# Kernel optimization log

Measured on AMD Instinct MI355X. Metric: run time of the kernel, lower is better.

## Reference

```python
import jax, jax.numpy as jnp
import numpy as np


def setup_inputs() -> dict:
    key = jax.random.key(0)
    k = jax.random.split(key, 6)
    B, S, d, n = 4, 4096, 1024, 64
    x = jax.random.normal(k[0], (B, S, d), dtype=jnp.float32)
    gate_W = jax.random.normal(k[1], (d, n), dtype=jnp.float32) / np.sqrt(d).astype(np.float32)
    gate_b = jnp.full((n,), 3.0, dtype=jnp.float32)  # nn.init.constant_(gate_proj.bias, 3.0)
    B_W = jax.random.normal(k[2], (d, n), dtype=jnp.float32) / np.sqrt(d).astype(np.float32)
    C_W = jax.random.normal(k[3], (n, d), dtype=jnp.float32) / np.sqrt(n).astype(np.float32)
    out_W = jax.random.normal(k[4], (d, d), dtype=jnp.float32) / np.sqrt(d).astype(np.float32)
    mix_weight = jnp.eye(n, dtype=jnp.float32) + 0.01 * jax.random.normal(k[5], (n, n), dtype=jnp.float32)
    return {"x": x, "gate_W": gate_W, "gate_b": gate_b, "B_W": B_W,
            "C_W": C_W, "out_W": out_W, "mix_weight": mix_weight, "chunk_size": 16}


def _ssm_forward(x, gate_W, gate_b, B_W, C_W, out_W, mix_weight, chunk_size):
    Bb, S, d = x.shape
    n = gate_W.shape[1]
    C = chunk_size
    K = S // C  # seq_len chosen divisible by chunk_size -> F.pad path is a no-op
    # Vectorized per-timestep projections (done once for the whole sequence)
    gates = jax.nn.sigmoid(jnp.einsum('bsd,dn->bsn', x, gate_W) + gate_b)  # a_t in (0,1)
    b_all = jnp.einsum('bsd,dn->bsn', x, B_W)
    a_ch = gates.reshape(Bb, K, C, n).transpose(1, 2, 0, 3)  # (K, C, B, n)
    b_ch = b_all.reshape(Bb, K, C, n).transpose(1, 2, 0, 3)

    def chunk_step(h_prev, ab):
        a_c, b_c = ab  # each (C, B, n)
        def step(h, t):
            a_t, b_t = t
            h = a_t * h + b_t
            return h, h
        h_final, h_stack = jax.lax.scan(step, h_prev, (a_c, b_c))  # h_stack: (C, B, n)
        gate_prod = jnp.prod(a_c, axis=0)  # (B, n) cumulative diag gates
        # T_chunk = mix @ diag(gate_prod): T[b,i,j] = mix[i,j] * gate_prod[b,j]
        T = mix_weight[None, :, :] * gate_prod[:, None, :]
        Th = jnp.einsum('bij,bj->bi', T, h_prev)
        b_chunk = h_final - Th
        h_next = Th + b_chunk  # canonical inter-chunk propagation: T @ h_prev + b_chunk
        return h_next, h_stack

    h0 = jnp.zeros((Bb, n), dtype=x.dtype)
    _, h_all = jax.lax.scan(chunk_step, h0, (a_ch, b_ch))  # (K, C, B, n)
    h_seq = h_all.transpose(2, 0, 1, 3).reshape(Bb, S, n)
    y = jnp.einsum('bsn,nd->bsd', h_seq, C_W)
    out_gate = jax.nn.sigmoid(jnp.einsum('bsd,de->bse', x, out_W))
    return y * out_gate


def reference(x, gate_W, gate_b, B_W, C_W, out_W, mix_weight, chunk_size):
    return _ssm_forward(x, gate_W, gate_b, B_W, C_W, out_W, mix_weight, chunk_size)
```

## Files before the change

### kernel.cpp

```cpp
#include <hip/hip_runtime.h>
#include <stdint.h>

typedef __attribute__((ext_vector_type(8))) short short8;
typedef __attribute__((ext_vector_type(4))) float f32x4;
typedef __attribute__((ext_vector_type(4))) float f4;
typedef __attribute__((ext_vector_type(4))) unsigned short us4;
typedef __attribute__((ext_vector_type(4))) unsigned int u32x4;

typedef unsigned short ushort_t;

__device__ __forceinline__ ushort_t f2bf(float f) {
    union { float f; uint32_t u; } c; c.f = f;
    uint32_t u = c.u;
    uint32_t r = u + 0x7fffu + ((u >> 16) & 1u);
    return (ushort_t)(r >> 16);
}
__device__ __forceinline__ float bf2f(ushort_t h) {
    union { uint32_t u; float f; } c; c.u = ((uint32_t)h) << 16;
    return c.f;
}
__device__ __forceinline__ uint32_t cvtpk(float lo, float hi) {
    uint32_t r;
    asm("v_cvt_pk_bf16_f32 %0, %1, %2" : "=v"(r) : "v"(lo), "v"(hi));
    return r;
}

typedef const __attribute__((address_space(1))) unsigned int as1_uint;
typedef __attribute__((address_space(3))) unsigned int as3_uint;
__device__ __forceinline__ void gload_lds16(const void* g, void* l) {
    __builtin_amdgcn_global_load_lds((as1_uint*)g, (as3_uint*)l, 16, 0, 0);
}

#define SWIDX(r, c) ((r) * 64 + ((c) ^ (((r) & 7) << 3)))

__global__ void prep_weights(const float* __restrict__ gate_W, const float* __restrict__ B_W,
                             const float* __restrict__ C_W, const float* __restrict__ out_W,
                             ushort_t* __restrict__ W1t_hi, ushort_t* __restrict__ W1t_lo,
                             ushort_t* __restrict__ outWt, ushort_t* __restrict__ Ct)
{
    int idx = blockIdx.x * 256 + threadIdx.x;
    int stride = gridDim.x * 256;
    for (int i = idx; i < 1024 * 1024; i += stride) {
        int nn = i >> 10, kk = i & 1023;
        outWt[i] = f2bf(out_W[kk * 1024 + nn]);
    }
    for (int i = idx; i < 128 * 1024; i += stride) {
        int nn = i >> 10, kk = i & 1023;
        float v = (nn < 64) ? gate_W[kk * 64 + nn] : B_W[kk * 64 + (nn - 64)];
        ushort_t h = f2bf(v);
        W1t_hi[i] = h;
        W1t_lo[i] = f2bf(v - bf2f(h));
    }
    for (int i = idx; i < 1024 * 64; i += stride) {
        int nn = i >> 6, kk = i & 63;
        Ct[i] = f2bf(C_W[kk * 1024 + nn]);
    }
}

__global__ __launch_bounds__(256, 2)
void p1_kernel(const float* __restrict__ x,
               const ushort_t* __restrict__ W1t_hi, const ushort_t* __restrict__ W1t_lo,
               ushort_t* __restrict__ x_hi, float* __restrict__ Zpart)
{
    __shared__ ushort_t Ash[128 * 64];
    __shared__ ushort_t Asl[128 * 64];
    __shared__ ushort_t Bsh[64 * 64];

    const int tid = threadIdx.x;
    const int wave = tid >> 6, lane = tid & 63;
    const int wm = wave >> 1, wn = wave & 1;
    const int s0 = blockIdx.x * 64;
    const int kc = blockIdx.y;

    f32x4 acc[4][2];
#pragma unroll
    for (int i = 0; i < 4; i++)
#pragma unroll
        for (int j = 0; j < 2; j++) { f32x4 z = {0.f,0.f,0.f,0.f}; acc[i][j] = z; }

    for (int kt = 0; kt < 8; ++kt) {
        const int k0 = kc * 512 + kt * 64;
#pragma unroll
        for (int p = 0; p < 4; ++p) {
            int c = p * 256 + wave * 64 + lane;
            int row = c >> 3, col = (c & 7) * 8;
            gload_lds16(W1t_hi + (size_t)row * 1024 + k0 + col,
                        &Ash[(p * 256 + wave * 64) * 8]);
            gload_lds16(W1t_lo + (size_t)row * 1024 + k0 + col,
                        &Asl[(p * 256 + wave * 64) * 8]);
        }
#pragma unroll
        for (int p = 0; p < 2; ++p) {
            int f = tid + p * 256;
            int row = f >> 3, col = (f & 7) * 8;
            const float* src = x + (size_t)(s0 + row) * 1024 + k0 + col;
            f4 v0 = *(const f4*)src;
            f4 v1 = *(const f4*)(src + 4);
            u32x4 pk = { cvtpk(v0[0], v0[1]), cvtpk(v0[2], v0[3]),
                         cvtpk(v1[0], v1[1]), cvtpk(v1[2], v1[3]) };
            *(u32x4*)&Bsh[row * 64 + col] = pk;
            *(u32x4*)(x_hi + (size_t)(s0 + row) * 1024 + k0 + col) = pk;
        }
        __syncthreads();
#pragma unroll
        for (int kk = 0; kk < 2; ++kk) {
            const int kb = kk * 32 + (lane >> 4) * 8;
            short8 ah[4], al[4], bh[2];
#pragma unroll
            for (int fm = 0; fm < 4; fm++) {
                int r = wm * 64 + fm * 16 + (lane & 15);
                ah[fm] = *(const short8*)&Ash[r * 64 + kb];
                al[fm] = *(const short8*)&Asl[r * 64 + kb];
            }
#pragma unroll
            for (int fn = 0; fn < 2; fn++) {
                int r = wn * 32 + fn * 16 + (lane & 15);
                bh[fn] = *(const short8*)&Bsh[r * 64 + kb];
            }
#pragma unroll
            for (int fm = 0; fm < 4; fm++)
#pragma unroll
                for (int fn = 0; fn < 2; fn++) {
                    acc[fm][fn] = __builtin_amdgcn_mfma_f32_16x16x32_bf16(ah[fm], bh[fn], acc[fm][fn], 0, 0, 0);
                    acc[fm][fn] = __builtin_amdgcn_mfma_f32_16x16x32_bf16(al[fm], bh[fn], acc[fm][fn], 0, 0, 0);
                }
        }
        __syncthreads();
    }
#pragma unroll
    for (int fm = 0; fm < 4; fm++) {
#pragma unroll
        for (int fn = 0; fn < 2; fn++) {
            int scol = s0 + wn * 32 + fn * 16 + (lane & 15);
            int b = scol >> 12, sb = scol & 4095;
            int nbase = wm * 64 + fm * 16 + ((lane >> 4) << 2);
#pragma unroll
            for (int r = 0; r < 4; r++) {
                Zpart[((size_t)kc * 512 + b * 128 + nbase + r) * 4096 + sb] = acc[fm][fn][r];
            }
        }
    }
}

__global__ __launch_bounds__(256)
void scan_kernel(const float* __restrict__ Zpart, const float* __restrict__ gate_b,
                 ushort_t* __restrict__ hT)
{
    __shared__ float SA[256], SB[256];
    const int bn = blockIdx.x;
    const int t = threadIdx.x;
    const int b = bn >> 6, n = bn & 63;
    const float gb = gate_b[n];
    const float* g0 = Zpart + ((size_t)(b * 128 + n)) * 4096;
    const float* g1 = g0 + (size_t)512 * 4096;
    const float* b0 = Zpart + ((size_t)(b * 128 + 64 + n)) * 4096;
    const float* b1 = b0 + (size_t)512 * 4096;
    const int sb = t * 16;

    float a[16], bb[16];
#pragma unroll
    for (int q = 0; q < 4; q++) {
        f4 vg0 = *(const f4*)(g0 + sb + q * 4);
        f4 vg1 = *(const f4*)(g1 + sb + q * 4);
        f4 vb0 = *(const f4*)(b0 + sb + q * 4);
        f4 vb1 = *(const f4*)(b1 + sb + q * 4);
#pragma unroll
        for (int j = 0; j < 4; j++) {
            a[q * 4 + j] = 1.f / (1.f + __expf(-(vg0[j] + vg1[j] + gb)));
            bb[q * 4 + j] = vb0[j] + vb1[j];
        }
    }
    float A = 1.f, Bv = 0.f;
#pragma unroll
    for (int i = 0; i < 16; i++) { Bv = a[i] * Bv + bb[i]; A *= a[i]; }
    SA[t] = A; SB[t] = Bv;
    __syncthreads();
    for (int off = 1; off < 256; off <<= 1) {
        float a1 = 1.f, b1v = 0.f;
        if (t >= off) { a1 = SA[t - off]; b1v = SB[t - off]; }
        float a2 = SA[t], b2 = SB[t];
        __syncthreads();
        SA[t] = a1 * a2;
        SB[t] = a2 * b1v + b2;
        __syncthreads();
    }
    float h = (t == 0) ? 0.f : SB[t - 1];
    float hv[16];
#pragma unroll
    for (int i = 0; i < 16; i++) {
        h = a[i] * h + bb[i];
        hv[i] = h;
    }
    ushort_t* dst = hT + (size_t)bn * 4096 + sb;
    u32x4 o0 = { cvtpk(hv[0], hv[1]),  cvtpk(hv[2], hv[3]),
                 cvtpk(hv[4], hv[5]),  cvtpk(hv[6], hv[7]) };
    u32x4 o1 = { cvtpk(hv[8], hv[9]),  cvtpk(hv[10], hv[11]),
                 cvtpk(hv[12], hv[13]), cvtpk(hv[14], hv[15]) };
    *(u32x4*)(dst)     = o0;
    *(u32x4*)(dst + 8) = o1;
}

__global__ __launch_bounds__(512, 2)
void gemm_out256(const ushort_t* __restrict__ x_hi, const ushort_t* __restrict__ outWt,
                 const ushort_t* __restrict__ hT, const ushort_t* __restrict__ Ct,
                 float* __restrict__ out)
{
    __shared__ ushort_t As[2][256 * 64];
    __shared__ ushort_t Bs[2][256 * 64];

    const int tid = threadIdx.x;
    const int wave = tid >> 6, lane = tid & 63;
    const int wm = wave >> 2;
    const int wn = wave & 3;

    const int flat = blockIdx.x;
    const int swz = (flat & 7) * 32 + (flat >> 3);
    const int m0 = (swz >> 2) * 256;
    const int n0 = (swz & 3) * 256;

    const int lcol0 = (lane >> 4) * 8;
    const int lrow = lane & 15;
    const int lxor = (lrow & 7) << 3;

    const int aOff0 = (wm * 32 + lrow) * 64 + (lcol0 ^ lxor);
    const int aOff1 = (wm * 32 + lrow) * 64 + ((32 + lcol0) ^ lxor);
    const int bOff0 = (wn * 64 + lrow) * 64 + (lcol0 ^ lxor);
    const int bOff1 = (wn * 64 + lrow) * 64 + ((32 + lcol0) ^ lxor);

    const int rl0 = tid >> 3;
    const int col0 = ((tid & 7) ^ (rl0 & 7)) << 3;
    const ushort_t* gB0a = outWt + (size_t)(n0 + rl0) * 1024 + col0;
    const ushort_t* gB0b = gB0a + 64 * 1024;
    const ushort_t* gB1a = outWt + (size_t)(n0 + 128 + rl0) * 1024 + col0;
    const ushort_t* gB1b = gB1a + 64 * 1024;
    const ushort_t* gA0a = x_hi + (size_t)(m0 + rl0) * 1024 + col0;
    const ushort_t* gA0b = gA0a + 64 * 1024;
    const ushort_t* gA1a = x_hi + (size_t)(m0 + 128 + rl0) * 1024 + col0;
    const ushort_t* gA1b = gA1a + 64 * 1024;

    auto STG = [&](const ushort_t*& ga, const ushort_t*& gb, ushort_t* ldsbase) {
        gload_lds16(ga, ldsbase + wave * 512);
        gload_lds16(gb, ldsbase + 4096 + wave * 512);
        ga += 64; gb += 64;
    };

    f32x4 acc[8][4];
#pragma unroll
    for (int i = 0; i < 8; i++)
#pragma unroll
        for (int j = 0; j < 4; j++) { f32x4 z = {0.f,0.f,0.f,0.f}; acc[i][j] = z; }

    STG(gB0a, gB0b, &Bs[0][0]);
    STG(gB1a, gB1b, &Bs[0][8192]);
    STG(gA0a, gA0b, &As[0][0]);
    STG(gA1a, gA1b, &As[0][8192]);
    asm volatile("s_waitcnt vmcnt(2)" ::: "memory");
    __builtin_amdgcn_s_barrier();

    short8 aR0[2][2], aR1[2][2], bfr[4][2];
#pragma unroll
    for (int mm = 0; mm < 2; ++mm) {
        aR0[mm][0] = *(const short8*)&As[0][aOff0 + mm * 1024];
        aR0[mm][1] = *(const short8*)&As[0][aOff1 + mm * 1024];
    }

#define MFMA_Q(q, AR)                                                              \
    do {                                                                           \
        __builtin_amdgcn_s_setprio(1);                                             \
        _Pragma("unroll") for (int mm = 0; mm < 2; ++mm)                           \
            _Pragma("unroll") for (int fn = 0; fn < 4; ++fn) {                     \
                acc[2*(q)+mm][fn] = __builtin_amdgcn_mfma_f32_16x16x32_bf16(       \
                    AR[mm][0], bfr[fn][0], acc[2*(q)+mm][fn], 0, 0, 0);            \
                acc[2*(q)+mm][fn] = __builtin_amdgcn_mfma_f32_16x16x32_bf16(       \
                    AR[mm][1], bfr[fn][1], acc[2*(q)+mm][fn], 0, 0, 0);            \
            }                                                                      \
        __builtin_amdgcn_s_setprio(0);                                             \
    } while (0)

    for (int t = 0; t < 16; ++t) {
        const int bc = t & 1;
        const ushort_t* as = &As[bc][0];
        const ushort_t* bs = &Bs[bc][0];
        const ushort_t* asn = &As[bc ^ 1][0];

        if (t < 15) STG(gB0a, gB0b, &Bs[bc ^ 1][0]);
#pragma unroll
        for (int fn = 0; fn < 4; ++fn) {
            bfr[fn][0] = *(const short8*)(bs + bOff0 + fn * 1024);
            bfr[fn][1] = *(const short8*)(bs + bOff1 + fn * 1024);
        }
#pragma unroll
        for (int mm = 0; mm < 2; ++mm) {
            aR1[mm][0] = *(const short8*)(as + aOff0 + 4096 + mm * 1024);
            aR1[mm][1] = *(const short8*)(as + aOff1 + 4096 + mm * 1024);
        }
        asm volatile("s_waitcnt lgkmcnt(4)" ::: "memory");
        __builtin_amdgcn_sched_barrier(0);
        MFMA_Q(0, aR0);
        if (t < 15) { asm volatile("s_waitcnt vmcnt(2)" ::: "memory"); }
        else        { asm volatile("s_waitcnt vmcnt(0)" ::: "memory"); }
        __builtin_amdgcn_s_barrier();

        if (t < 15) {
            STG(gB1a, gB1b, &Bs[bc ^ 1][8192]);
            STG(gA0a, gA0b, &As[bc ^ 1][0]);
        }
#pragma unroll
        for (int mm = 0; mm < 2; ++mm) {
            aR0[mm][0] = *(const short8*)(as + aOff0 + 2 * 4096 + mm * 1024);
            aR0[mm][1] = *(const short8*)(as + aOff1 + 2 * 4096 + mm * 1024);
        }
        asm volatile("s_waitcnt lgkmcnt(4)" ::: "memory");
        __builtin_amdgcn_sched_barrier(0);
        MFMA_Q(1, aR1);
        __builtin_amdgcn_s_barrier();

        if (t < 15) STG(gA1a, gA1b, &As[bc ^ 1][8192]);
#pragma unroll
        for (int mm = 0; mm < 2; ++mm) {
            aR1[mm][0] = *(const short8*)(as + aOff0 + 3 * 4096 + mm * 1024);
            aR1[mm][1] = *(const short8*)(as + aOff1 + 3 * 4096 + mm * 1024);
        }
        asm volatile("s_waitcnt lgkmcnt(4)" ::: "memory");
        __builtin_amdgcn_sched_barrier(0);
        MFMA_Q(2, aR0);
        if (t < 15) { asm volatile("s_waitcnt vmcnt(2)" ::: "memory"); }
        __builtin_amdgcn_s_barrier();

        if (t < 15) {
#pragma unroll
            for (int mm = 0; mm < 2; ++mm) {
                aR0[mm][0] = *(const short8*)(asn + aOff0 + mm * 1024);
                aR0[mm][1] = *(const short8*)(asn + aOff1 + mm * 1024);
            }
            asm volatile("s_waitcnt lgkmcnt(4)" ::: "memory");
        } else {
            asm volatile("s_waitcnt lgkmcnt(0)" ::: "memory");
        }
        __builtin_amdgcn_sched_barrier(0);
        MFMA_Q(3, aR1);
        __builtin_amdgcn_s_barrier();
    }
#undef MFMA_Q

    const int b64 = (m0 >> 12) * 64;
    const int sb0 = m0 & 4095;
#pragma unroll
    for (int p = 0; p < 4; ++p) {
        int c = p * 512 + wave * 64 + lane;
        int row = c >> 3;
        int col = (((c & 7) ^ (row & 7)) << 3);
        gload_lds16(Ct + (size_t)(n0 + row) * 64 + col,
                    &Bs[0][(p * 512 + wave * 64) * 8]);
    }
#pragma unroll
    for (int p = 0; p < 4; ++p) {
        int c = tid + p * 512;
        int kn = c & 63, mc = c >> 6;
        short8 v = *(const short8*)(hT + (size_t)(b64 + kn) * 4096 + sb0 + mc * 8);
#pragma unroll
        for (int j = 0; j < 8; ++j)
            As[0][SWIDX(mc * 8 + j, kn)] = (ushort_t)v[j];
    }
    __syncthreads();

    short8 by[4][2];
#pragma unroll
    for (int fn = 0; fn < 4; fn++)
#pragma unroll
        for (int kk = 0; kk < 2; kk++) {
            int r = wn * 64 + fn * 16 + lrow;
            by[fn][kk] = *(const short8*)&Bs[0][SWIDX(r, kk * 32 + lcol0)];
        }

#pragma unroll
    for (int g = 0; g < 4; g++) {
        f32x4 ty[2][4];
#pragma unroll
        for (int mm = 0; mm < 2; mm++)
#pragma unroll
            for (int fn = 0; fn < 4; fn++) { f32x4 z = {0.f,0.f,0.f,0.f}; ty[mm][fn] = z; }
#pragma unroll
        for (int mm = 0; mm < 2; mm++) {
            int r = g * 64 + wm * 32 + mm * 16 + lrow;
            short8 a0 = *(const short8*)&As[0][SWIDX(r, lcol0)];
            short8 a1 = *(const short8*)&As[0][SWIDX(r, 32 + lcol0)];
#pragma unroll
            for (int fn = 0; fn < 4; fn++) {
                ty[mm][fn] = __builtin_amdgcn_mfma_f32_16x16x32_bf16(a0, by[fn][0], ty[mm][fn], 0, 0, 0);
                ty[mm][fn] = __builtin_amdgcn_mfma_f32_16x16x32_bf16(a1, by[fn][1], ty[mm][fn], 0, 0, 0);
            }
        }
#pragma unroll
        for (int mm = 0; mm < 2; mm++)
#pragma unroll
            for (int fn = 0; fn < 4; fn++) {
                int col = n0 + wn * 64 + fn * 16 + lrow;
                int rbase = m0 + g * 64 + wm * 32 + mm * 16 + ((lane >> 4) << 2);
#pragma unroll
                for (int r = 0; r < 4; r++) {
                    float og = 1.f / (1.f + __expf(-acc[g * 2 + mm][fn][r]));
                    out[(size_t)(rbase + r) * 1024 + col] = ty[mm][fn][r] * og;
                }
            }
    }
}

extern "C" void kernel_launch(void* const* d_in, const int* in_sizes, int n_in,
                              void* d_out, int out_size, void* d_ws, size_t ws_size,
                              hipStream_t stream)
{
    const float* x      = (const float*)d_in[0];
    const float* gate_W = (const float*)d_in[1];
    const float* gate_b = (const float*)d_in[2];
    const float* B_W    = (const float*)d_in[3];
    const float* C_W    = (const float*)d_in[4];
    const float* out_W  = (const float*)d_in[5];
    float* out = (float*)d_out;

    char* ws = (char*)d_ws;
    float*    Zpart  = (float*)(ws + 0);
    ushort_t* hT     = (ushort_t*)(ws + 16777216);
    ushort_t* x_hi   = (ushort_t*)(ws + 18874368);
    ushort_t* W1t_hi = (ushort_t*)(ws + 52428800);
    ushort_t* W1t_lo = (ushort_t*)(ws + 52690944);
    ushort_t* outWt  = (ushort_t*)(ws + 52953088);
    ushort_t* Ct     = (ushort_t*)(ws + 55050240);

    prep_weights<<<512, 256, 0, stream>>>(gate_W, B_W, C_W, out_W,
                                          W1t_hi, W1t_lo, outWt, Ct);

    p1_kernel<<<dim3(256, 2), 256, 0, stream>>>(x, W1t_hi, W1t_lo, x_hi, Zpart);

    scan_kernel<<<256, 256, 0, stream>>>(Zpart, gate_b, hT);

    gemm_out256<<<256, 512, 0, stream>>>(x_hi, outWt, hT, Ct, out);
}
```

Before: 83.49 us.

## Drop split-K in projection GEMM and transpose out_W via shared-memory tiles

The projection kernel no longer splits K across two block columns. Each block now covers 32 sequence rows over the full K range, so the scan kernel reads one partial sum per gate and B value instead of adding two. Separately, the out_W transpose and bf16 conversion moves into its own kernel that goes through LDS tiles, replacing the strided global reads of the old grid-stride loop. The trade-off is that each projection block re-streams the full weight panel for half as many rows, which raises weight traffic per output row.

Result: slower. 89.85 us, median of 2 (+7.6%).

```diff
diff --git a/kernel.cpp b/kernel.cpp
--- a/kernel.cpp
+++ b/kernel.cpp
@@ -34,16 +34,12 @@
 #define SWIDX(r, c) ((r) * 64 + ((c) ^ (((r) & 7) << 3)))
 
 __global__ void prep_weights(const float* __restrict__ gate_W, const float* __restrict__ B_W,
-                             const float* __restrict__ C_W, const float* __restrict__ out_W,
+                             const float* __restrict__ C_W,
                              ushort_t* __restrict__ W1t_hi, ushort_t* __restrict__ W1t_lo,
-                             ushort_t* __restrict__ outWt, ushort_t* __restrict__ Ct)
+                             ushort_t* __restrict__ Ct)
 {
     int idx = blockIdx.x * 256 + threadIdx.x;
     int stride = gridDim.x * 256;
-    for (int i = idx; i < 1024 * 1024; i += stride) {
-        int nn = i >> 10, kk = i & 1023;
-        outWt[i] = f2bf(out_W[kk * 1024 + nn]);
-    }
     for (int i = idx; i < 128 * 1024; i += stride) {
         int nn = i >> 10, kk = i & 1023;
         float v = (nn < 64) ? gate_W[kk * 64 + nn] : B_W[kk * 64 + (nn - 64)];
@@ -57,6 +53,31 @@
     }
 }
 
+__global__ __launch_bounds__(256)
+void prep_outwt(const float* __restrict__ out_W, ushort_t* __restrict__ outWt)
+{
+    __shared__ ushort_t T[64][65];
+    const int kk0 = blockIdx.x * 64, nn0 = blockIdx.y * 64;
+    const int tid = threadIdx.x;
+#pragma unroll
+    for (int p = 0; p < 16; ++p) {
+        int r = p * 4 + (tid >> 6);
+        int c = tid & 63;
+        T[c][r] = f2bf(out_W[(size_t)(kk0 + r) * 1024 + nn0 + c]);
+    }
+    __syncthreads();
+#pragma unroll
+    for (int p = 0; p < 2; ++p) {
+        int idx = tid + p * 256;
+        int r = idx >> 3;
+        int cc = (idx & 7) * 8;
+        short8 v;
+#pragma unroll
+        for (int j = 0; j < 8; ++j) v[j] = (short)T[r][cc + j];
+        *(short8*)(outWt + (size_t)(nn0 + r) * 1024 + kk0 + cc) = v;
+    }
+}
+
 __global__ __launch_bounds__(256, 2)
 void p1_kernel(const float* __restrict__ x,
                const ushort_t* __restrict__ W1t_hi, const ushort_t* __restrict__ W1t_lo,
@@ -64,22 +85,19 @@
 {
     __shared__ ushort_t Ash[128 * 64];
     __shared__ ushort_t Asl[128 * 64];
-    __shared__ ushort_t Bsh[64 * 64];
+    __shared__ ushort_t Bsh[32 * 64];
 
     const int tid = threadIdx.x;
     const int wave = tid >> 6, lane = tid & 63;
     const int wm = wave >> 1, wn = wave & 1;
-    const int s0 = blockIdx.x * 64;
-    const int kc = blockIdx.y;
-
-    f32x4 acc[4][2];
-#pragma unroll
-    for (int i = 0; i < 4; i++)
-#pragma unroll
-        for (int j = 0; j < 2; j++) { f32x4 z = {0.f,0.f,0.f,0.f}; acc[i][j] = z; }
-
-    for (int kt = 0; kt < 8; ++kt) {
-        const int k0 = kc * 512 + kt * 64;
+    const int s0 = blockIdx.x * 32;
+
+    f32x4 acc[4];
+#pragma unroll
+    for (int i = 0; i < 4; i++) { f32x4 z = {0.f,0.f,0.f,0.f}; acc[i] = z; }
+
+    for (int kt = 0; kt < 16; ++kt) {
+        const int k0 = kt * 64;
 #pragma unroll
         for (int p = 0; p < 4; ++p) {
             int c = p * 256 + wave * 64 + lane;
@@ -89,10 +107,8 @@
             gload_lds16(W1t_lo + (size_t)row * 1024 + k0 + col,
                         &Asl[(p * 256 + wave * 64) * 8]);
         }
-#pragma unroll
-        for (int p = 0; p < 2; ++p) {
-            int f = tid + p * 256;
-            int row = f >> 3, col = (f & 7) * 8;
+        {
+            int row = tid >> 3, col = (tid & 7) * 8;
             const float* src = x + (size_t)(s0 + row) * 1024 + k0 + col;
             f4 v0 = *(const f4*)src;
             f4 v1 = *(const f4*)(src + 4);
@@ -105,39 +121,33 @@
 #pragma unroll
         for (int kk = 0; kk < 2; ++kk) {
             const int kb = kk * 32 + (lane >> 4) * 8;
-            short8 ah[4], al[4], bh[2];
+            short8 ah[4], al[4], bh;
 #pragma unroll
             for (int fm = 0; fm < 4; fm++) {
                 int r = wm * 64 + fm * 16 + (lane & 15);
                 ah[fm] = *(const short8*)&Ash[r * 64 + kb];
                 al[fm] = *(const short8*)&Asl[r * 64 + kb];
             }
-#pragma unroll
-            for (int fn = 0; fn < 2; fn++) {
-                int r = wn * 32 + fn * 16 + (lane & 15);
-                bh[fn] = *(const short8*)&Bsh[r * 64 + kb];
-            }
-#pragma unroll
-            for (int fm = 0; fm < 4; fm++)
-#pragma unroll
-                for (int fn = 0; fn < 2; fn++) {
-                    acc[fm][fn] = __builtin_amdgcn_mfma_f32_16x16x32_bf16(ah[fm], bh[fn], acc[fm][fn], 0, 0, 0);
-                    acc[fm][fn] = __builtin_amdgcn_mfma_f32_16x16x32_bf16(al[fm], bh[fn], acc[fm][fn], 0, 0, 0);
-                }
+            {
+                int r = wn * 16 + (lane & 15);
+                bh = *(const short8*)&Bsh[r * 64 + kb];
+            }
+#pragma unroll
+            for (int fm = 0; fm < 4; fm++) {
+                acc[fm] = __builtin_amdgcn_mfma_f32_16x16x32_bf16(ah[fm], bh, acc[fm], 0, 0, 0);
+                acc[fm] = __builtin_amdgcn_mfma_f32_16x16x32_bf16(al[fm], bh, acc[fm], 0, 0, 0);
+            }
         }
         __syncthreads();
     }
 #pragma unroll
     for (int fm = 0; fm < 4; fm++) {
-#pragma unroll
-        for (int fn = 0; fn < 2; fn++) {
-            int scol = s0 + wn * 32 + fn * 16 + (lane & 15);
-            int b = scol >> 12, sb = scol & 4095;
-            int nbase = wm * 64 + fm * 16 + ((lane >> 4) << 2);
-#pragma unroll
-            for (int r = 0; r < 4; r++) {
-                Zpart[((size_t)kc * 512 + b * 128 + nbase + r) * 4096 + sb] = acc[fm][fn][r];
-            }
+        int scol = s0 + wn * 16 + (lane & 15);
+        int b = scol >> 12, sb = scol & 4095;
+        int nbase = wm * 64 + fm * 16 + ((lane >> 4) << 2);
+#pragma unroll
+        for (int r = 0; r < 4; r++) {
+            Zpart[((size_t)(b * 128 + nbase + r)) * 4096 + sb] = acc[fm][r];
         }
     }
 }
@@ -152,22 +162,18 @@
     const int b = bn >> 6, n = bn & 63;
     const float gb = gate_b[n];
     const float* g0 = Zpart + ((size_t)(b * 128 + n)) * 4096;
-    const float* g1 = g0 + (size_t)512 * 4096;
     const float* b0 = Zpart + ((size_t)(b * 128 + 64 + n)) * 4096;
-    const float* b1 = b0 + (size_t)512 * 4096;
     const int sb = t * 16;
 
     float a[16], bb[16];
 #pragma unroll
     for (int q = 0; q < 4; q++) {
         f4 vg0 = *(const f4*)(g0 + sb + q * 4);
-        f4 vg1 = *(const f4*)(g1 + sb + q * 4);
         f4 vb0 = *(const f4*)(b0 + sb + q * 4);
-        f4 vb1 = *(const f4*)(b1 + sb + q * 4);
 #pragma unroll
         for (int j = 0; j < 4; j++) {
-            a[q * 4 + j] = 1.f / (1.f + __expf(-(vg0[j] + vg1[j] + gb)));
-            bb[q * 4 + j] = vb0[j] + vb1[j];
+            a[q * 4 + j] = 1.f / (1.f + __expf(-(vg0[j] + gb)));
+            bb[q * 4 + j] = vb0[j];
         }
     }
     float A = 1.f, Bv = 0.f;
@@ -427,10 +433,10 @@
     ushort_t* outWt  = (ushort_t*)(ws + 52953088);
     ushort_t* Ct     = (ushort_t*)(ws + 55050240);
 
-    prep_weights<<<512, 256, 0, stream>>>(gate_W, B_W, C_W, out_W,
-                                          W1t_hi, W1t_lo, outWt, Ct);
-
-    p1_kernel<<<dim3(256, 2), 256, 0, stream>>>(x, W1t_hi, W1t_lo, x_hi, Zpart);
+    prep_weights<<<64, 256, 0, stream>>>(gate_W, B_W, C_W, W1t_hi, W1t_lo, Ct);
+    prep_outwt<<<dim3(16, 16), 256, 0, stream>>>(out_W, outWt);
+
+    p1_kernel<<<512, 256, 0, stream>>>(x, W1t_hi, W1t_lo, x_hi, Zpart);
 
     scan_kernel<<<256, 256, 0, stream>>>(Zpart, gate_b, hT);
 
```
